# Kernel tuning notes

Measured on AMD Instinct MI355X. Metric: run time of the kernel, lower is better.

## Reference

```python
import jax, jax.numpy as jnp
import numpy as np

D_MODEL = 1024
HEAD_SIZE = 64
BLOCK_SIZE = 2048
B, T = 4, 2048


def setup_inputs() -> dict:
    key = jax.random.key(0)
    ks = jax.random.split(key, 7)
    s = 1.0 / np.sqrt(D_MODEL)
    x = jax.random.normal(ks[0], (B, T, D_MODEL), dtype=jnp.float32)
    Wq = jax.random.uniform(ks[1], (D_MODEL, HEAD_SIZE), jnp.float32, -s, s)
    bq = jax.random.uniform(ks[2], (HEAD_SIZE,), jnp.float32, -s, s)
    Wk = jax.random.uniform(ks[3], (D_MODEL, HEAD_SIZE), jnp.float32, -s, s)
    bk = jax.random.uniform(ks[4], (HEAD_SIZE,), jnp.float32, -s, s)
    Wv = jax.random.uniform(ks[5], (D_MODEL, HEAD_SIZE), jnp.float32, -s, s)
    return {"x": x, "Wq": Wq, "bq": bq, "Wk": Wk, "bk": bk, "Wv": Wv, "mask": 1}


def reference(x, Wq, bq, Wk, bk, Wv, mask):
    # x: [B, T, C]; single attention head, dropout is identity (eval/p=0)
    Tlen = x.shape[1]
    q = x @ Wq + bq              # [B, T, hs]
    k = x @ Wk + bk              # [B, T, hs]
    v = x @ Wv                   # [B, T, hs] (no bias)
    hs = k.shape[-1]
    # Faithful to source: weights = QK^T / hs**(-0.5)  ==  QK^T * sqrt(hs)
    w = jnp.einsum('btd,bsd->bts', q, k) * jnp.sqrt(jnp.asarray(hs, x.dtype))
    if mask:
        causal = jnp.tril(jnp.ones((Tlen, Tlen), dtype=bool))
        w = jnp.where(causal, w, jnp.asarray(-jnp.inf, w.dtype))
    w = jax.nn.softmax(w, axis=-1)
    out = jnp.einsum('bts,bsd->btd', w, v)  # [B, T, hs]
    return out
```

## Files before the change

kernel.cpp:

```cpp
#include <hip/hip_runtime.h>
#include <hip/hip_bf16.h>

#define D_MODEL 1024
#define HS 64
#define T_LEN 2048
#define JCH 512
#define NCH 4

typedef __attribute__((ext_vector_type(8))) short bf16x8;
typedef __attribute__((ext_vector_type(4))) float f32x4;

__device__ inline void split8(const float* v, int4& hi, int4& lo) {
    union { unsigned short u[8]; int4 v4; } uh, ul;
    #pragma unroll
    for (int i = 0; i < 8; ++i) {
        const unsigned int b = __float_as_uint(v[i]);
        const unsigned short h = (unsigned short)(b >> 16);
        const float r = v[i] - __uint_as_float((unsigned int)h << 16);
        uh.u[i] = h;
        ul.u[i] = (unsigned short)(__float_as_uint(r) >> 16);
    }
    hi = uh.v4; lo = ul.v4;
}

__device__ inline unsigned short f2bf_rne(float f) {
    const unsigned int b = __float_as_uint(f);
    return (unsigned short)((b + 0x7FFFu + ((b >> 16) & 1u)) >> 16);
}
__device__ inline float bf2f(unsigned short h) {
    return __uint_as_float((unsigned int)h << 16);
}

__global__ __launch_bounds__(256) void wprep_kernel(
    const float* __restrict__ Wq, const float* __restrict__ Wk,
    const float* __restrict__ Wv, short* __restrict__ Wh, short* __restrict__ Wl)
{
    __shared__ float tile[64][69];
    const int tid = threadIdx.x;
    const int kb = blockIdx.x & 15;
    const int m  = blockIdx.x >> 4;
    const float* W = (m == 0) ? Wq : (m == 1) ? Wk : Wv;
    #pragma unroll
    for (int it = 0; it < 4; ++it) {
        const int idx = tid + 256 * it;
        const int kr = idx >> 4, c4 = idx & 15;
        *(float4*)&tile[kr][4 * c4] =
            *(const float4*)(W + (size_t)(kb * 64 + kr) * HS + 4 * c4);
    }
    __syncthreads();
    #pragma unroll
    for (int it = 0; it < 2; ++it) {
        const int s = tid + 256 * it;
        const int n = s >> 3, kc = s & 7;
        float v[8];
        #pragma unroll
        for (int i = 0; i < 8; ++i) v[i] = tile[kc * 8 + i][n];
        int4 hi, lo;
        split8(v, hi, lo);
        const size_t off = (size_t)(m * 64 + n) * D_MODEL + kb * 64 + kc * 8;
        *(int4*)(Wh + off) = hi;
        *(int4*)(Wl + off) = lo;
    }
}

__global__ __launch_bounds__(256, 2) void qkv_kernel(
    const float* __restrict__ x,
    const short* __restrict__ Wh, const short* __restrict__ Wl,
    const float* __restrict__ bq, const float* __restrict__ bk,
    float* __restrict__ q, float* __restrict__ k, float* __restrict__ vt, int BT)
{
    __shared__ __align__(16) short Ah[2 * 520], Al[2 * 520];
    __shared__ __align__(16) short Bh[4 * 520], Bl[4 * 520];

    const int tid  = threadIdx.x;
    const int r0   = blockIdx.x * 32;
    const int nb   = blockIdx.y;
    const int wave = tid >> 6;
    const int lane = tid & 63;
    const int mt_w = wave >> 1;
    const int nt0  = (wave & 1) * 2;

    f32x4 acc0 = (f32x4)(0.f);
    f32x4 acc1 = (f32x4)(0.f);

    const bool doA = (tid >= 128);
    const int  au  = tid & 127;
    const int  amt = au >> 6;
    const int  aln = au & 63;
    const float* axsrc =
        x + (size_t)(r0 + amt * 16 + (aln & 15)) * D_MODEL + (aln >> 4) * 8;

    const int bnt = tid >> 6;
    const int bln = tid & 63;
    const size_t boff =
        (size_t)(nb * 64 + bnt * 16 + (bln & 15)) * D_MODEL + (bln >> 4) * 8;

    float4 a0v, a1v;
    int4 pbh, pbl;
    if (doA) {
        a0v = *(const float4*)(axsrc);
        a1v = *(const float4*)(axsrc + 4);
    }
    pbh = *(const int4*)(Wh + boff);
    pbl = *(const int4*)(Wl + boff);

    for (int k0 = 0; k0 < D_MODEL; k0 += 32) {
        __syncthreads();
        if (doA) {
            float xv[8];
            *(float4*)&xv[0] = a0v;
            *(float4*)&xv[4] = a1v;
            int4 hi, lo;
            split8(xv, hi, lo);
            *(int4*)&Ah[amt * 520 + aln * 8] = hi;
            *(int4*)&Al[amt * 520 + aln * 8] = lo;
        }
        *(int4*)&Bh[bnt * 520 + bln * 8] = pbh;
        *(int4*)&Bl[bnt * 520 + bln * 8] = pbl;
        __syncthreads();
        const int kn = k0 + 32;
        if (kn < D_MODEL) {
            if (doA) {
                a0v = *(const float4*)(axsrc + kn);
                a1v = *(const float4*)(axsrc + kn + 4);
            }
            pbh = *(const int4*)(Wh + boff + kn);
            pbl = *(const int4*)(Wl + boff + kn);
        }
        const bf16x8 afh = *(const bf16x8*)&Ah[mt_w * 520 + lane * 8];
        const bf16x8 afl = *(const bf16x8*)&Al[mt_w * 520 + lane * 8];
        {
            const bf16x8 bfh = *(const bf16x8*)&Bh[nt0 * 520 + lane * 8];
            const bf16x8 bfl = *(const bf16x8*)&Bl[nt0 * 520 + lane * 8];
            acc0 = __builtin_amdgcn_mfma_f32_16x16x32_bf16(afh, bfh, acc0, 0, 0, 0);
            acc0 = __builtin_amdgcn_mfma_f32_16x16x32_bf16(afh, bfl, acc0, 0, 0, 0);
            acc0 = __builtin_amdgcn_mfma_f32_16x16x32_bf16(afl, bfh, acc0, 0, 0, 0);
        }
        {
            const bf16x8 bfh = *(const bf16x8*)&Bh[(nt0 + 1) * 520 + lane * 8];
            const bf16x8 bfl = *(const bf16x8*)&Bl[(nt0 + 1) * 520 + lane * 8];
            acc1 = __builtin_amdgcn_mfma_f32_16x16x32_bf16(afh, bfh, acc1, 0, 0, 0);
            acc1 = __builtin_amdgcn_mfma_f32_16x16x32_bf16(afh, bfl, acc1, 0, 0, 0);
            acc1 = __builtin_amdgcn_mfma_f32_16x16x32_bf16(afl, bfh, acc1, 0, 0, 0);
        }
    }

    const int rowb = r0 + mt_w * 16 + (lane >> 4) * 4;
    #pragma unroll
    for (int j = 0; j < 2; ++j) {
        const f32x4 a = (j == 0) ? acc0 : acc1;
        const int c = nb * 64 + (nt0 + j) * 16 + (lane & 15);
        if (c < 64) {
            const float bias = bq[c];
            #pragma unroll
            for (int r = 0; r < 4; ++r)
                q[(size_t)(rowb + r) * HS + c] = a[r] + bias;
        } else if (c < 128) {
            const float bias = bk[c - 64];
            #pragma unroll
            for (int r = 0; r < 4; ++r)
                k[(size_t)(rowb + r) * HS + (c - 64)] = a[r] + bias;
        } else {
            float4 o;
            o.x = a[0]; o.y = a[1]; o.z = a[2]; o.w = a[3];
            *(float4*)(vt + (size_t)(c - 128) * BT + rowb) = o;
        }
    }
}

__global__ __launch_bounds__(256) void attn_kernel(
    const float* __restrict__ q_ws, const float* __restrict__ k_ws,
    const float* __restrict__ vt_ws, const int* __restrict__ maskp,
    float* __restrict__ part_O, float* __restrict__ part_ml, int BT)
{
    __shared__ __align__(16) short Kh[4096], Kl[4096];
    __shared__ __align__(16) short Vt[4096];
    __shared__ __align__(16) short Pl[4][16 * 72];

    const int tile  = blockIdx.x;
    const int chunk = blockIdx.y;
    const int r0 = tile * 64;
    const int tb = r0 / T_LEN;
    const int t0 = r0 - tb * T_LEN;
    const int mask = (*maskp != 0);
    const int n_max = mask ? (t0 + 64) : T_LEN;
    const int j0 = chunk * JCH;
    if (j0 >= n_max) return;
    const int hi_j = min(j0 + JCH, n_max);
    const int njt = (hi_j - j0 + 63) >> 6;

    const int tid  = threadIdx.x;
    const int w    = tid >> 6;
    const int lane = tid & 63;
    const int quad = lane >> 4;
    const int l15  = lane & 15;
    const int rw0  = t0 + 16 * w;
    const int rowa = r0 + 16 * w + quad * 4;

    bf16x8 qfh[2], qfl[2];
    {
        const float* qrow = q_ws + (size_t)(r0 + 16 * w + l15) * HS + quad * 8;
        #pragma unroll
        for (int kc = 0; kc < 2; ++kc) {
            float v[8];
            *(float4*)&v[0] = *(const float4*)(qrow + kc * 32);
            *(float4*)&v[4] = *(const float4*)(qrow + kc * 32 + 4);
            union { int4 i; bf16x8 b; } ch, cl;
            split8(v, ch.i, cl.i);
            qfh[kc] = ch.b;
            qfl[kc] = cl.b;
        }
    }

    f32x4 oacc[4];
    #pragma unroll
    for (int nt = 0; nt < 4; ++nt) oacc[nt] = (f32x4)(0.f);
    float m_r[4] = {-INFINITY, -INFINITY, -INFINITY, -INFINITY};
    float l_r[4] = {0.f, 0.f, 0.f, 0.f};

    const float* kbase = k_ws + (size_t)tb * T_LEN * HS;

    for (int jt = 0; jt < njt; ++jt) {
        const int jbase = j0 + jt * 64;
        __syncthreads();
        #pragma unroll
        for (int it = 0; it < 2; ++it) {
            const int s  = tid + 256 * it;
            const int ls = s & 63;
            const int sc = s >> 6;
            const int jsub = sc >> 1, kc = sc & 1;
            const int jrow = jbase + jsub * 16 + (ls & 15);
            const int koff = kc * 32 + (ls >> 4) * 8;
            const float* src = kbase + (size_t)jrow * HS + koff;
            float v[8];
            *(float4*)&v[0] = *(const float4*)src;
            *(float4*)&v[4] = *(const float4*)(src + 4);
            int4 hi, lo;
            split8(v, hi, lo);
            *(int4*)&Kh[s * 8] = hi;
            *(int4*)&Kl[s * 8] = lo;
        }
        #pragma unroll
        for (int it = 0; it < 2; ++it) {
            const int s  = tid + 256 * it;
            const int ls = s & 63;
            const int sc = s >> 6;
            const int jc = sc >> 2, nt = sc & 3;
            const int n  = nt * 16 + (ls & 15);
            const int jcol = jbase + jc * 32 + (ls >> 4) * 8;
            const float* src = vt_ws + (size_t)n * BT + tb * T_LEN + jcol;
            float v[8];
            *(float4*)&v[0] = *(const float4*)src;
            *(float4*)&v[4] = *(const float4*)(src + 4);
            union { unsigned short u[8]; int4 i; } pk;
            #pragma unroll
            for (int i = 0; i < 8; ++i) pk.u[i] = f2bf_rne(v[i]);
            *(int4*)&Vt[s * 8] = pk.i;
        }
        __syncthreads();

        const bool active = (!mask) || (jbase <= rw0 + 15);
        if (active) {
            f32x4 sacc[4];
            #pragma unroll
            for (int jsub = 0; jsub < 4; ++jsub) {
                f32x4 s = (f32x4)(0.f);
                #pragma unroll
                for (int kc = 0; kc < 2; ++kc) {
                    const bf16x8 kh = *(const bf16x8*)&Kh[((jsub * 2 + kc) * 64 + lane) * 8];
                    const bf16x8 kl = *(const bf16x8*)&Kl[((jsub * 2 + kc) * 64 + lane) * 8];
                    s = __builtin_amdgcn_mfma_f32_16x16x32_bf16(qfh[kc], kh, s, 0, 0, 0);
                    s = __builtin_amdgcn_mfma_f32_16x16x32_bf16(qfh[kc], kl, s, 0, 0, 0);
                    s = __builtin_amdgcn_mfma_f32_16x16x32_bf16(qfl[kc], kh, s, 0, 0, 0);
                }
                sacc[jsub] = s;
            }
            float sval[4][4], rmax[4];
            #pragma unroll
            for (int r = 0; r < 4; ++r) rmax[r] = -INFINITY;
            #pragma unroll
            for (int jsub = 0; jsub < 4; ++jsub) {
                const int jg = jbase + jsub * 16 + l15;
                #pragma unroll
                for (int r = 0; r < 4; ++r) {
                    const int tg = rw0 + quad * 4 + r;
                    const float vv = (mask && (jg > tg)) ? -INFINITY : 8.0f * sacc[jsub][r];
                    sval[jsub][r] = vv;
                    rmax[r] = fmaxf(rmax[r], vv);
                }
            }
            #pragma unroll
            for (int d = 1; d < 16; d <<= 1)
                #pragma unroll
                for (int r = 0; r < 4; ++r)
                    rmax[r] = fmaxf(rmax[r], __shfl_xor(rmax[r], d));
            float alpha[4], msafe[4];
            #pragma unroll
            for (int r = 0; r < 4; ++r) {
                const float mn = fmaxf(m_r[r], rmax[r]);
                msafe[r] = (mn == -INFINITY) ? 0.f : mn;
                alpha[r] = __expf(m_r[r] - msafe[r]);
                m_r[r] = mn;
            }
            short* Pw = &Pl[w][0];
            float rsum[4] = {0.f, 0.f, 0.f, 0.f};
            #pragma unroll
            for (int jsub = 0; jsub < 4; ++jsub) {
                #pragma unroll
                for (int r = 0; r < 4; ++r) {
                    const float e = __expf(sval[jsub][r] - msafe[r]);
                    const unsigned short eb = f2bf_rne(e);
                    Pw[(quad * 4 + r) * 72 + jsub * 16 + l15] = (short)eb;
                    rsum[r] += bf2f(eb);
                }
            }
            #pragma unroll
            for (int d = 1; d < 16; d <<= 1)
                #pragma unroll
                for (int r = 0; r < 4; ++r)
                    rsum[r] += __shfl_xor(rsum[r], d);
            #pragma unroll
            for (int r = 0; r < 4; ++r)
                l_r[r] = l_r[r] * alpha[r] + rsum[r];
            #pragma unroll
            for (int nt = 0; nt < 4; ++nt)
                #pragma unroll
                for (int r = 0; r < 4; ++r)
                    oacc[nt][r] *= alpha[r];
            bf16x8 pf[2];
            #pragma unroll
            for (int jc = 0; jc < 2; ++jc)
                pf[jc] = *(const bf16x8*)&Pw[l15 * 72 + jc * 32 + quad * 8];
            #pragma unroll
            for (int nt = 0; nt < 4; ++nt) {
                #pragma unroll
                for (int jc = 0; jc < 2; ++jc) {
                    const bf16x8 vf = *(const bf16x8*)&Vt[((jc * 4 + nt) * 64 + lane) * 8];
                    oacc[nt] = __builtin_amdgcn_mfma_f32_16x16x32_bf16(pf[jc], vf, oacc[nt], 0, 0, 0);
                }
            }
        }
    }

    #pragma unroll
    for (int nt = 0; nt < 4; ++nt)
        #pragma unroll
        for (int r = 0; r < 4; ++r)
            part_O[((size_t)(rowa + r) * NCH + chunk) * HS + nt * 16 + l15] = oacc[nt][r];
    if (l15 == 0) {
        #pragma unroll
        for (int r = 0; r < 4; ++r) {
            float2 ml;
            ml.x = m_r[r];
            ml.y = l_r[r];
            *(float2*)(part_ml + ((size_t)(rowa + r) * NCH + chunk) * 2) = ml;
        }
    }
}

__global__ __launch_bounds__(256) void combine_kernel(
    const float* __restrict__ part_O, const float* __restrict__ part_ml,
    const int* __restrict__ maskp, float* __restrict__ out)
{
    const int f = blockIdx.x * 256 + threadIdx.x;
    const int row = f >> 6;
    const int d = f & 63;
    const int t = row & (T_LEN - 1);
    const int mask = (*maskp != 0);
    const int n = mask ? (t + 1) : T_LEN;
    const int nc = (n + JCH - 1) / JCH;

    float mv[NCH], lv[NCH];
    float M = -INFINITY;
    for (int c = 0; c < nc; ++c) {
        const float2 ml = *(const float2*)(part_ml + ((size_t)row * NCH + c) * 2);
        mv[c] = ml.x; lv[c] = ml.y;
        M = fmaxf(M, ml.x);
    }
    float L = 0.f, O = 0.f;
    for (int c = 0; c < nc; ++c) {
        const float w = __expf(mv[c] - M);
        L += lv[c] * w;
        O = fmaf(part_O[((size_t)row * NCH + c) * HS + d], w, O);
    }
    out[(size_t)row * HS + d] = O / L;
}

extern "C" void kernel_launch(void* const* d_in, const int* in_sizes, int n_in,
                              void* d_out, int out_size, void* d_ws, size_t ws_size,
                              hipStream_t stream) {
    const float* x  = (const float*)d_in[0];
    const float* Wq = (const float*)d_in[1];
    const float* bq = (const float*)d_in[2];
    const float* Wk = (const float*)d_in[3];
    const float* bk = (const float*)d_in[4];
    const float* Wv = (const float*)d_in[5];
    const int* maskp = (const int*)d_in[6];

    const int BT = in_sizes[0] / D_MODEL;

    float* q   = (float*)d_ws;
    float* k   = q + (size_t)BT * HS;
    float* vt  = k + (size_t)BT * HS;
    float* pO  = vt + (size_t)BT * HS;
    float* pml = pO + (size_t)BT * NCH * HS;

    short* Wh = (short*)pO;
    short* Wl = Wh + (size_t)192 * D_MODEL;

    wprep_kernel<<<48, 256, 0, stream>>>(Wq, Wk, Wv, Wh, Wl);
    dim3 qgrid(BT / 32, 3);
    qkv_kernel<<<qgrid, 256, 0, stream>>>(x, Wh, Wl, bq, bk, q, k, vt, BT);
    dim3 agrid(BT / 64, NCH);
    attn_kernel<<<agrid, 256, 0, stream>>>(q, k, vt, maskp, pO, pml, BT);
    combine_kernel<<<(BT * HS) / 256, 256, 0, stream>>>(pO, pml, maskp, (float*)d_out);
}
```

Before: 151.2 us.

## Halve attention chunk size, double QKV k-step to 64, simplify combine

The attention split-KV chunk shrinks from 512 to 256 keys, giving twice as many chunks per row. The aim is more parallel work and better load balance across the causal triangle, at the cost of more partial outputs for the combine step. The QKV projection kernel now stages 64 k-elements per iteration with all threads loading, which halves the number of barrier pairs, and it raises the occupancy hint to 3. The combine kernel rereads the partial max and sum values from memory instead of holding them in per-thread arrays, which saves registers.

```diff
diff --git a/kernel.cpp b/kernel.cpp
--- a/kernel.cpp
+++ b/kernel.cpp
@@ -4,8 +4,8 @@
 #define D_MODEL 1024
 #define HS 64
 #define T_LEN 2048
-#define JCH 512
-#define NCH 4
+#define JCH 256
+#define NCH 8
 
 typedef __attribute__((ext_vector_type(8))) short bf16x8;
 typedef __attribute__((ext_vector_type(4))) float f32x4;
@@ -63,14 +63,14 @@
     }
 }
 
-__global__ __launch_bounds__(256, 2) void qkv_kernel(
+__global__ __launch_bounds__(256, 3) void qkv_kernel(
     const float* __restrict__ x,
     const short* __restrict__ Wh, const short* __restrict__ Wl,
     const float* __restrict__ bq, const float* __restrict__ bk,
     float* __restrict__ q, float* __restrict__ k, float* __restrict__ vt, int BT)
 {
-    __shared__ __align__(16) short Ah[2 * 520], Al[2 * 520];
-    __shared__ __align__(16) short Bh[4 * 520], Bl[4 * 520];
+    __shared__ __align__(16) short Ah[4 * 520], Al[4 * 520];
+    __shared__ __align__(16) short Bh[8 * 520], Bl[8 * 520];
 
     const int tid  = threadIdx.x;
     const int r0   = blockIdx.x * 32;
@@ -83,65 +83,67 @@
     f32x4 acc0 = (f32x4)(0.f);
     f32x4 acc1 = (f32x4)(0.f);
 
-    const bool doA = (tid >= 128);
-    const int  au  = tid & 127;
-    const int  amt = au >> 6;
-    const int  aln = au & 63;
+    const int amt = tid >> 7, akc = (tid >> 6) & 1, aln = tid & 63;
     const float* axsrc =
-        x + (size_t)(r0 + amt * 16 + (aln & 15)) * D_MODEL + (aln >> 4) * 8;
-
-    const int bnt = tid >> 6;
-    const int bln = tid & 63;
-    const size_t boff =
-        (size_t)(nb * 64 + bnt * 16 + (bln & 15)) * D_MODEL + (bln >> 4) * 8;
-
-    float4 a0v, a1v;
-    int4 pbh, pbl;
-    if (doA) {
-        a0v = *(const float4*)(axsrc);
-        a1v = *(const float4*)(axsrc + 4);
-    }
-    pbh = *(const int4*)(Wh + boff);
-    pbl = *(const int4*)(Wl + boff);
-
-    for (int k0 = 0; k0 < D_MODEL; k0 += 32) {
+        x + (size_t)(r0 + amt * 16 + (aln & 15)) * D_MODEL + akc * 32 + (aln >> 4) * 8;
+
+    const int b0nt = tid >> 7, b0kc = (tid >> 6) & 1, b0ln = tid & 63;
+    const size_t b0off =
+        (size_t)(nb * 64 + b0nt * 16 + (b0ln & 15)) * D_MODEL + b0kc * 32 + (b0ln >> 4) * 8;
+    const int b1nt = 2 + (tid >> 7);
+    const size_t b1off =
+        (size_t)(nb * 64 + b1nt * 16 + (b0ln & 15)) * D_MODEL + b0kc * 32 + (b0ln >> 4) * 8;
+
+    float4 a0v = *(const float4*)(axsrc);
+    float4 a1v = *(const float4*)(axsrc + 4);
+    int4 pb0h = *(const int4*)(Wh + b0off);
+    int4 pb0l = *(const int4*)(Wl + b0off);
+    int4 pb1h = *(const int4*)(Wh + b1off);
+    int4 pb1l = *(const int4*)(Wl + b1off);
+
+    for (int k0 = 0; k0 < D_MODEL; k0 += 64) {
         __syncthreads();
-        if (doA) {
+        {
             float xv[8];
             *(float4*)&xv[0] = a0v;
             *(float4*)&xv[4] = a1v;
             int4 hi, lo;
             split8(xv, hi, lo);
-            *(int4*)&Ah[amt * 520 + aln * 8] = hi;
-            *(int4*)&Al[amt * 520 + aln * 8] = lo;
-        }
-        *(int4*)&Bh[bnt * 520 + bln * 8] = pbh;
-        *(int4*)&Bl[bnt * 520 + bln * 8] = pbl;
+            *(int4*)&Ah[(amt * 2 + akc) * 520 + aln * 8] = hi;
+            *(int4*)&Al[(amt * 2 + akc) * 520 + aln * 8] = lo;
+        }
+        *(int4*)&Bh[(b0nt * 2 + b0kc) * 520 + b0ln * 8] = pb0h;
+        *(int4*)&Bl[(b0nt * 2 + b0kc) * 520 + b0ln * 8] = pb0l;
+        *(int4*)&Bh[(b1nt * 2 + b0kc) * 520 + b0ln * 8] = pb1h;
+        *(int4*)&Bl[(b1nt * 2 + b0kc) * 520 + b0ln * 8] = pb1l;
         __syncthreads();
-        const int kn = k0 + 32;
+        const int kn = k0 + 64;
         if (kn < D_MODEL) {
-            if (doA) {
-                a0v = *(const float4*)(axsrc + kn);
-                a1v = *(const float4*)(axsrc + kn + 4);
-            }
-            pbh = *(const int4*)(Wh + boff + kn);
-            pbl = *(const int4*)(Wl + boff + kn);
-        }
-        const bf16x8 afh = *(const bf16x8*)&Ah[mt_w * 520 + lane * 8];
-        const bf16x8 afl = *(const bf16x8*)&Al[mt_w * 520 + lane * 8];
-        {
-            const bf16x8 bfh = *(const bf16x8*)&Bh[nt0 * 520 + lane * 8];
-            const bf16x8 bfl = *(const bf16x8*)&Bl[nt0 * 520 + lane * 8];
-            acc0 = __builtin_amdgcn_mfma_f32_16x16x32_bf16(afh, bfh, acc0, 0, 0, 0);
-            acc0 = __builtin_amdgcn_mfma_f32_16x16x32_bf16(afh, bfl, acc0, 0, 0, 0);
-            acc0 = __builtin_amdgcn_mfma_f32_16x16x32_bf16(afl, bfh, acc0, 0, 0, 0);
-        }
-        {
-            const bf16x8 bfh = *(const bf16x8*)&Bh[(nt0 + 1) * 520 + lane * 8];
-            const bf16x8 bfl = *(const bf16x8*)&Bl[(nt0 + 1) * 520 + lane * 8];
-            acc1 = __builtin_amdgcn_mfma_f32_16x16x32_bf16(afh, bfh, acc1, 0, 0, 0);
-            acc1 = __builtin_amdgcn_mfma_f32_16x16x32_bf16(afh, bfl, acc1, 0, 0, 0);
-            acc1 = __builtin_amdgcn_mfma_f32_16x16x32_bf16(afl, bfh, acc1, 0, 0, 0);
+            a0v = *(const float4*)(axsrc + kn);
+            a1v = *(const float4*)(axsrc + kn + 4);
+            pb0h = *(const int4*)(Wh + b0off + kn);
+            pb0l = *(const int4*)(Wl + b0off + kn);
+            pb1h = *(const int4*)(Wh + b1off + kn);
+            pb1l = *(const int4*)(Wl + b1off + kn);
+        }
+        #pragma unroll
+        for (int kc = 0; kc < 2; ++kc) {
+            const bf16x8 afh = *(const bf16x8*)&Ah[(mt_w * 2 + kc) * 520 + lane * 8];
+            const bf16x8 afl = *(const bf16x8*)&Al[(mt_w * 2 + kc) * 520 + lane * 8];
+            {
+                const bf16x8 bfh = *(const bf16x8*)&Bh[(nt0 * 2 + kc) * 520 + lane * 8];
+                const bf16x8 bfl = *(const bf16x8*)&Bl[(nt0 * 2 + kc) * 520 + lane * 8];
+                acc0 = __builtin_amdgcn_mfma_f32_16x16x32_bf16(afh, bfh, acc0, 0, 0, 0);
+                acc0 = __builtin_amdgcn_mfma_f32_16x16x32_bf16(afh, bfl, acc0, 0, 0, 0);
+                acc0 = __builtin_amdgcn_mfma_f32_16x16x32_bf16(afl, bfh, acc0, 0, 0, 0);
+            }
+            {
+                const bf16x8 bfh = *(const bf16x8*)&Bh[((nt0 + 1) * 2 + kc) * 520 + lane * 8];
+                const bf16x8 bfl = *(const bf16x8*)&Bl[((nt0 + 1) * 2 + kc) * 520 + lane * 8];
+                acc1 = __builtin_amdgcn_mfma_f32_16x16x32_bf16(afh, bfh, acc1, 0, 0, 0);
+                acc1 = __builtin_amdgcn_mfma_f32_16x16x32_bf16(afh, bfl, acc1, 0, 0, 0);
+                acc1 = __builtin_amdgcn_mfma_f32_16x16x32_bf16(afl, bfh, acc1, 0, 0, 0);
+            }
         }
     }
 
@@ -370,17 +372,14 @@
     const int n = mask ? (t + 1) : T_LEN;
     const int nc = (n + JCH - 1) / JCH;
 
-    float mv[NCH], lv[NCH];
+    const float2* mlp = (const float2*)(part_ml + (size_t)row * NCH * 2);
     float M = -INFINITY;
-    for (int c = 0; c < nc; ++c) {
-        const float2 ml = *(const float2*)(part_ml + ((size_t)row * NCH + c) * 2);
-        mv[c] = ml.x; lv[c] = ml.y;
-        M = fmaxf(M, ml.x);
-    }
+    for (int c = 0; c < nc; ++c) M = fmaxf(M, mlp[c].x);
     float L = 0.f, O = 0.f;
     for (int c = 0; c < nc; ++c) {
-        const float w = __expf(mv[c] - M);
-        L += lv[c] * w;
+        const float2 ml = mlp[c];
+        const float w = __expf(ml.x - M);
+        L += ml.y * w;
         O = fmaf(part_O[((size_t)row * NCH + c) * HS + d], w, O);
     }
     out[(size_t)row * HS + d] = O / L;
```

After: 155.2 us. +2.7%, slower.
